# Kernel tuning notes

Measured on AMD Instinct MI355X. Metric: run time of the kernel, lower is better.

## Reference

```python
import jax, jax.numpy as jnp
import numpy as np

B_, S_, P_, D_ = 2, 512, 64, 1024
L_ = 4            # n_layer
DI_ = 2 * D_      # d_inner (expand=2)
DS_ = 16          # d_state
DC_ = 4           # d_conv
DR_ = D_ // 16    # dt_rank
PCD_ = 768        # prepend_cond_dim


def setup_inputs() -> dict:
    key = jax.random.key(0)
    ks = jax.random.split(key, 12)
    n = lambda k, s, sc=0.02: jax.random.normal(k, s, dtype=jnp.float32) * sc
    A_log = jnp.log(jnp.broadcast_to(jnp.arange(1, DS_ + 1, dtype=jnp.float32), (L_, DI_, DS_)))
    return {
        'x': jax.random.normal(ks[0], (B_, S_, D_), dtype=jnp.float32),
        'prepend_cond': jax.random.normal(ks[1], (B_, P_, PCD_), dtype=jnp.float32),
        'pre_w1': n(ks[2], (PCD_, D_)),
        'pre_w2': n(ks[3], (D_, D_)),
        'norm_w': jnp.ones((L_, D_), jnp.float32),
        'in_proj_w': n(ks[4], (L_, 2 * DI_, D_)),
        'conv_w': n(ks[5], (L_, DI_, DC_), 0.1),
        'conv_b': jnp.zeros((L_, DI_), jnp.float32),
        'x_proj_w': n(ks[6], (L_, DR_ + 2 * DS_, DI_)),
        'dt_proj_w': n(ks[7], (L_, DI_, DR_), 0.1),
        'dt_proj_b': jax.random.uniform(ks[8], (L_, DI_), jnp.float32, -4.0, -2.0),
        'A_log': A_log,
        'D_param': jnp.ones((L_, DI_), jnp.float32),
        'out_proj_w': n(ks[9], (L_, D_, DI_)),
        'final_norm_w': jnp.ones((D_,), jnp.float32),
    }


def rmsnorm(x, w, eps=1e-5):
    return x * jax.lax.rsqrt(jnp.mean(x * x, axis=-1, keepdims=True) + eps) * w


def mamba_block(x, ip_w, cw, cb, xp_w, dtp_w, dtp_b, A_log, Dp, op_w):
    B, S, _ = x.shape
    xz = jnp.einsum('bsd,ed->bse', x, ip_w)            # [B,S,2*DI]
    xi, z = jnp.split(xz, 2, axis=-1)
    # depthwise causal conv1d along time
    xt = xi.transpose(0, 2, 1)                          # [B,DI,S]
    conv = jax.lax.conv_general_dilated(
        xt, cw[:, None, :], (1,), [(DC_ - 1, 0)], feature_group_count=DI_) + cb[:, None]
    xi = jax.nn.silu(conv.transpose(0, 2, 1))           # [B,S,DI]
    xdbl = jnp.einsum('bse,fe->bsf', xi, xp_w)          # [B,S,DR+2*DS]
    dt, Bm, Cm = jnp.split(xdbl, [DR_, DR_ + DS_], axis=-1)
    dt = jax.nn.softplus(jnp.einsum('bsr,er->bse', dt, dtp_w) + dtp_b)  # [B,S,DI]
    A = -jnp.exp(A_log)                                 # [DI,DS]
    dA = jnp.exp(dt[..., None] * A)                     # [B,S,DI,DS]
    dBu = dt[..., None] * Bm[:, :, None, :] * xi[..., None]

    def step(h, t):
        da, dbu, c = t
        h = da * h + dbu                                # [B,DI,DS]
        return h, jnp.einsum('bes,bs->be', h, c)

    h0 = jnp.zeros((B, DI_, DS_), x.dtype)
    _, ys = jax.lax.scan(step, h0, (dA.transpose(1, 0, 2, 3), dBu.transpose(1, 0, 2, 3), Cm.transpose(1, 0, 2)))
    y = ys.transpose(1, 0, 2) + xi * Dp
    y = y * jax.nn.silu(z)
    return jnp.einsum('bse,de->bsd', y, op_w)


def reference(x, prepend_cond, pre_w1, pre_w2, norm_w, in_proj_w, conv_w, conv_b,
              x_proj_w, dt_proj_w, dt_proj_b, A_log, D_param, out_proj_w, final_norm_w):
    p = jax.nn.silu(prepend_cond @ pre_w1) @ pre_w2     # to_prepend_embed
    h = jnp.concatenate([p, x], axis=1)                 # [B, P+S, D]
    for l in range(L_):
        h = h + mamba_block(rmsnorm(h, norm_w[l]), in_proj_w[l], conv_w[l], conv_b[l],
                            x_proj_w[l], dt_proj_w[l], dt_proj_b[l], A_log[l],
                            D_param[l], out_proj_w[l])
    h = rmsnorm(h, final_norm_w)
    return h[:, P_:, :]
```

## Files before the change

kernel.cpp:

```cpp
#include <hip/hip_runtime.h>
#include <math.h>

#define B_ 2
#define S_ 512
#define P_ 64
#define T_ 576
#define D_ 1024
#define L_ 4
#define DI_ 2048
#define DS_ 16
#define DC_ 4
#define DR_ 64
#define PCD_ 768
#define M_ (B_*T_)
#define CCH 18
#define NC (T_/CCH)
#define XKS 16
#define OPK 4

#define N_IP (2*DI_*D_/4)
#define N_XP (96*DI_/4)
#define N_DTP (DI_*DR_/4)
#define N_OP (D_*DI_/4)
#define CVB ((N_IP + N_XP + N_DTP + N_OP + 255) / 256)
#define SETSZ ((size_t)2*DI_*D_ + 96*DI_ + DI_*DR_ + D_*DI_)

typedef __attribute__((ext_vector_type(8))) short bf16x8;
typedef __attribute__((ext_vector_type(4))) float f32x4;

__device__ __forceinline__ float silu_f(float v) { return v / (1.f + __expf(-v)); }
__device__ __forceinline__ float softplus_f(float v) {
    return fmaxf(v, 0.f) + log1pf(__expf(-fabsf(v)));
}
__device__ __forceinline__ unsigned short bf16_rne(float x) {
    unsigned int b = __float_as_uint(x);
    b += 0x7fffu + ((b >> 16) & 1u);
    return (unsigned short)(b >> 16);
}
__device__ __forceinline__ float bf16_to_f(unsigned short u) {
    return __uint_as_float((unsigned int)u << 16);
}

typedef const void __attribute__((address_space(1)))* gas_t;
typedef void __attribute__((address_space(3)))* las_t;
__device__ __forceinline__ void async16(const void* g, void* l) {
    __builtin_amdgcn_global_load_lds((gas_t)g, (las_t)l, 16, 0, 0);
}

__device__ __forceinline__ void cvt4_body(int i,
    const float* s0, unsigned short* d0, int n0,
    const float* s1, unsigned short* d1, int n1,
    const float* s2, unsigned short* d2, int n2,
    const float* s3, unsigned short* d3, int n3)
{
    const float* s; unsigned short* d; int off;
    if (i < n0)                     { s = s0; d = d0; off = i; }
    else if (i < n0 + n1)           { s = s1; d = d1; off = i - n0; }
    else if (i < n0 + n1 + n2)      { s = s2; d = d2; off = i - n0 - n1; }
    else if (i < n0 + n1 + n2 + n3) { s = s3; d = d3; off = i - n0 - n1 - n2; }
    else return;
    const float4 v = ((const float4*)s)[off];
    ushort4 o;
    o.x = bf16_rne(v.x); o.y = bf16_rne(v.y);
    o.z = bf16_rne(v.z); o.w = bf16_rne(v.w);
    ((ushort4*)d)[off] = o;
}

template<int EPI, int BN>
__global__ __launch_bounds__(256) void gemm_mfma_kernel(
    const unsigned short* __restrict__ A, const unsigned short* __restrict__ W,
    float* __restrict__ C, float* __restrict__ C2,
    int M, int N, int K, int Kchunk)
{
    constexpr int NF = BN / 32;
    __shared__ unsigned short As[128 * 32];
    __shared__ unsigned short Bs[BN * 32];
    const int tid = threadIdx.x;
    const int wave = tid >> 6;
    const int lane = tid & 63;
    const int m0 = blockIdx.y * 128, n0 = blockIdx.x * BN;
    const int kbase = blockIdx.z * Kchunk;
    const int wm = (wave >> 1) * 64, wn = (wave & 1) * (BN / 2);

    const int srow = (wave << 5) + (lane >> 2);
    const int selem = (lane & 3) * 8;
    const unsigned short* gA = A + (size_t)(m0 + srow) * K + kbase + selem;
    const unsigned short* gB = W + (size_t)(n0 + srow) * K + kbase + selem;
    unsigned short* lA = As + (wave << 5) * 32;
    unsigned short* lB = Bs + (wave << 5) * 32;

    f32x4 acc[4][NF];
    #pragma unroll
    for (int i = 0; i < 4; ++i)
        #pragma unroll
        for (int j = 0; j < NF; ++j)
            acc[i][j] = (f32x4){0.f, 0.f, 0.f, 0.f};

    const int fr = lane & 15;
    const int fq = lane >> 4;
    const int aoff = (wm + fr) * 32 + fq * 8;
    const int boff = (wn + fr) * 32 + fq * 8;

    for (int k0 = 0; k0 < Kchunk; k0 += 32) {
        async16(gA, lA);
        async16(gA + (size_t)16 * K, lA + 16 * 32);
        if (BN == 128 || wave < BN / 32) {
            async16(gB, lB);
            async16(gB + (size_t)16 * K, lB + 16 * 32);
        }
        gA += 32; gB += 32;
        __syncthreads();
        bf16x8 af[4], bf[NF];
        #pragma unroll
        for (int i = 0; i < 4; ++i) af[i] = *(const bf16x8*)&As[aoff + i * 512];
        #pragma unroll
        for (int j = 0; j < NF; ++j) bf[j] = *(const bf16x8*)&Bs[boff + j * 512];
        #pragma unroll
        for (int i = 0; i < 4; ++i)
            #pragma unroll
            for (int j = 0; j < NF; ++j)
                acc[i][j] = __builtin_amdgcn_mfma_f32_16x16x32_bf16(
                    af[i], bf[j], acc[i][j], 0, 0, 0);
        __syncthreads();
    }

    #pragma unroll
    for (int i = 0; i < 4; ++i) {
        const int m = m0 + wm + i * 16 + fq * 4;
        #pragma unroll
        for (int j = 0; j < NF; ++j) {
            const int n = n0 + wn + j * 16 + fr;
            if (EPI == 6) {
                float* p = C + ((size_t)blockIdx.z * M + m) * N + n;
                #pragma unroll
                for (int r = 0; r < 4; ++r)
                    p[(size_t)r * N] = acc[i][j][r];
            } else if (EPI == 8) {
                unsigned short* p = (unsigned short*)C +
                                    ((size_t)blockIdx.z * M + m) * N + n;
                #pragma unroll
                for (int r = 0; r < 4; ++r)
                    p[(size_t)r * N] = bf16_rne(acc[i][j][r]);
            } else if (EPI == 7) {
                if (n < DI_) {
                    unsigned short* p = (unsigned short*)C + (size_t)m * DI_ + n;
                    #pragma unroll
                    for (int r = 0; r < 4; ++r)
                        p[(size_t)r * DI_] = bf16_rne(acc[i][j][r]);
                } else {
                    unsigned short* p = (unsigned short*)C2 + (size_t)m * DI_ + (n - DI_);
                    #pragma unroll
                    for (int r = 0; r < 4; ++r)
                        p[(size_t)r * DI_] = bf16_rne(silu_f(acc[i][j][r]));
                }
            }
        }
    }
}

__global__ __launch_bounds__(256) void xproj_mfma_kernel(
    const unsigned short* __restrict__ A,
    const unsigned short* __restrict__ W,
    float* __restrict__ P)
{
    __shared__ unsigned short As[128 * 32];
    __shared__ unsigned short Bs[96 * 32];
    const int tid = threadIdx.x;
    const int wave = tid >> 6;
    const int lane = tid & 63;
    const int m0 = blockIdx.y * 128;
    const int kbase = blockIdx.x * (DI_ / XKS);
    const int wm = (wave >> 1) * 64, wn = (wave & 1) * 48;

    const int srow = (wave << 5) + (lane >> 2);
    const int selem = (lane & 3) * 8;
    const unsigned short* gA = A + (size_t)(m0 + srow) * DI_ + kbase + selem;
    const unsigned short* gB = W + (size_t)srow * DI_ + kbase + selem;
    unsigned short* lA = As + (wave << 5) * 32;
    unsigned short* lB = Bs + (wave << 5) * 32;

    f32x4 acc[4][3];
    #pragma unroll
    for (int i = 0; i < 4; ++i)
        #pragma unroll
        for (int j = 0; j < 3; ++j)
            acc[i][j] = (f32x4){0.f, 0.f, 0.f, 0.f};

    const int fr = lane & 15;
    const int fq = lane >> 4;
    const int aoff = (wm + fr) * 32 + fq * 8;
    const int boff = (wn + fr) * 32 + fq * 8;

    #pragma unroll
    for (int kk = 0; kk < 4; ++kk) {
        async16(gA, lA);
        async16(gA + (size_t)16 * DI_, lA + 16 * 32);
        if (wave < 3) {
            async16(gB, lB);
            async16(gB + (size_t)16 * DI_, lB + 16 * 32);
        }
        gA += 32; gB += 32;
        __syncthreads();
        bf16x8 af[4], bf[3];
        #pragma unroll
        for (int i = 0; i < 4; ++i) af[i] = *(const bf16x8*)&As[aoff + i * 512];
        #pragma unroll
        for (int j = 0; j < 3; ++j) bf[j] = *(const bf16x8*)&Bs[boff + j * 512];
        #pragma unroll
        for (int i = 0; i < 4; ++i)
            #pragma unroll
            for (int j = 0; j < 3; ++j)
                acc[i][j] = __builtin_amdgcn_mfma_f32_16x16x32_bf16(
                    af[i], bf[j], acc[i][j], 0, 0, 0);
        __syncthreads();
    }

    float* Pb = P + ((size_t)blockIdx.x * M_ + m0) * 96;
    #pragma unroll
    for (int i = 0; i < 4; ++i) {
        const int m = wm + i * 16 + fq * 4;
        #pragma unroll
        for (int j = 0; j < 3; ++j) {
            const int n = wn + j * 16 + fr;
            #pragma unroll
            for (int r = 0; r < 4; ++r)
                Pb[(size_t)(m + r) * 96 + n] = acc[i][j][r];
        }
    }
}

__global__ __launch_bounds__(256) void xproj_reduce_kernel(
    const float* __restrict__ P, float* __restrict__ Bc, float* __restrict__ Cc,
    unsigned short* __restrict__ dtr_bf)
{
    const int i = blockIdx.x * 256 + threadIdx.x;
    if (i >= M_ * 96) return;
    float s = 0.f;
    #pragma unroll
    for (int ks = 0; ks < XKS; ++ks) s += P[(size_t)ks * (M_ * 96) + i];
    const int m = i / 96;
    const int n = i - m * 96;
    if (n < DR_)            dtr_bf[(size_t)m * DR_ + n] = bf16_rne(s);
    else if (n < DR_ + DS_) Bc[(size_t)m * DS_ + (n - DR_)] = s;
    else                    Cc[(size_t)m * DS_ + (n - DR_ - DS_)] = s;
}

__global__ __launch_bounds__(256) void cvt_bf16_kernel(
    const float* __restrict__ in, unsigned short* __restrict__ out, int n4)
{
    const int i = blockIdx.x * 256 + threadIdx.x;
    if (i >= n4) return;
    const float4 v = ((const float4*)in)[i];
    ushort4 o;
    o.x = bf16_rne(v.x); o.y = bf16_rne(v.y);
    o.z = bf16_rne(v.z); o.w = bf16_rne(v.w);
    ((ushort4*)out)[i] = o;
}

__global__ __launch_bounds__(256) void cvt_transpose_kernel(
    const float* __restrict__ in, unsigned short* __restrict__ out, int K, int N)
{
    __shared__ float t[64][65];
    const int k0 = blockIdx.x * 64;
    const int n0 = blockIdx.y * 64;
    const int tx = threadIdx.x & 63;
    const int ty = threadIdx.x >> 6;
    #pragma unroll
    for (int j = 0; j < 16; ++j) {
        const int kk = ty * 16 + j;
        t[kk][tx] = in[(size_t)(k0 + kk) * N + n0 + tx];
    }
    __syncthreads();
    #pragma unroll
    for (int j = 0; j < 16; ++j) {
        const int nn = ty * 16 + j;
        out[(size_t)(n0 + nn) * K + k0 + tx] = bf16_rne(t[tx][nn]);
    }
}

__global__ __launch_bounds__(256) void reduce_silu_bf16_kernel(
    const float* __restrict__ P, unsigned short* __restrict__ o, int MN, int ns)
{
    const int i = blockIdx.x * 256 + threadIdx.x;
    if (i >= MN) return;
    float s = 0.f;
    for (int k = 0; k < ns; ++k) s += P[(size_t)k * MN + i];
    o[i] = bf16_rne(silu_f(s));
}
__global__ __launch_bounds__(256) void reduce_fp32_kernel(
    const float* __restrict__ P, float* __restrict__ o, int MN, int ns)
{
    const int i = blockIdx.x * 256 + threadIdx.x;
    if (i >= MN) return;
    float s = 0.f;
    for (int k = 0; k < ns; ++k) s += P[(size_t)k * MN + i];
    o[i] = s;
}

__global__ __launch_bounds__(256) void outproj_rmsnorm_cvt_kernel(
    const unsigned short* __restrict__ P, float* __restrict__ h,
    const float* __restrict__ w, unsigned short* __restrict__ outb, int donorm,
    const float* s0, unsigned short* d0, int n0,
    const float* s1, unsigned short* d1, int n1,
    const float* s2, unsigned short* d2, int n2,
    const float* s3, unsigned short* d3, int n3)
{
    const int bid = blockIdx.x;
    if (bid >= M_) {
        cvt4_body((bid - M_) * 256 + threadIdx.x,
                  s0, d0, n0, s1, d1, n1, s2, d2, n2, s3, d3, n3);
        return;
    }
    const int r = bid;
    const int i = r * 256 + threadIdx.x;
    float4 v = ((float4*)h)[i];
    #pragma unroll
    for (int k = 0; k < OPK; ++k) {
        const ushort4 a4 = ((const ushort4*)P)[(size_t)k * (M_ * D_ / 4) + i];
        v.x += bf16_to_f(a4.x); v.y += bf16_to_f(a4.y);
        v.z += bf16_to_f(a4.z); v.w += bf16_to_f(a4.w);
    }
    ((float4*)h)[i] = v;
    if (!donorm) return;
    float ss = v.x * v.x + v.y * v.y + v.z * v.z + v.w * v.w;
    ss += __shfl_xor(ss, 32, 64);
    ss += __shfl_xor(ss, 16, 64);
    ss += __shfl_xor(ss, 8, 64);
    ss += __shfl_xor(ss, 4, 64);
    ss += __shfl_xor(ss, 2, 64);
    ss += __shfl_xor(ss, 1, 64);
    __shared__ float red[4];
    if ((threadIdx.x & 63) == 0) red[threadIdx.x >> 6] = ss;
    __syncthreads();
    const float tot = red[0] + red[1] + red[2] + red[3];
    const float scale = rsqrtf(tot * (1.f / D_) + 1e-5f);
    const float4 wv = ((const float4*)w)[threadIdx.x];
    ushort4 o;
    o.x = bf16_rne(v.x * scale * wv.x);
    o.y = bf16_rne(v.y * scale * wv.y);
    o.z = bf16_rne(v.z * scale * wv.z);
    o.w = bf16_rne(v.w * scale * wv.w);
    ((ushort4*)(outb + (size_t)r * D_))[threadIdx.x] = o;
}

__global__ __launch_bounds__(256) void assemble_h_kernel(
    const float* __restrict__ p, const float* __restrict__ x, float* __restrict__ h)
{
    const int idx = blockIdx.x * 256 + threadIdx.x;
    const int r = idx >> 8;
    const int c = idx & 255;
    const int b = r / T_;
    const int t = r - b * T_;
    float4 v;
    if (t < P_) v = ((const float4*)p)[(size_t)(b * P_ + t) * 256 + c];
    else        v = ((const float4*)x)[(size_t)(b * S_ + (t - P_)) * 256 + c];
    ((float4*)h)[idx] = v;
}

__global__ __launch_bounds__(256) void rmsnorm_cvt_kernel(
    const float* __restrict__ x, const float* __restrict__ w,
    unsigned short* __restrict__ outb,
    const float* s0, unsigned short* d0, int n0,
    const float* s1, unsigned short* d1, int n1,
    const float* s2, unsigned short* d2, int n2,
    const float* s3, unsigned short* d3, int n3)
{
    const int bid = blockIdx.x;
    if (bid >= M_) {
        cvt4_body((bid - M_) * 256 + threadIdx.x,
                  s0, d0, n0, s1, d1, n1, s2, d2, n2, s3, d3, n3);
        return;
    }
    const int r = bid;
    const float4 v = ((const float4*)(x + (size_t)r * D_))[threadIdx.x];
    float ss = v.x * v.x + v.y * v.y + v.z * v.z + v.w * v.w;
    ss += __shfl_xor(ss, 32, 64);
    ss += __shfl_xor(ss, 16, 64);
    ss += __shfl_xor(ss, 8, 64);
    ss += __shfl_xor(ss, 4, 64);
    ss += __shfl_xor(ss, 2, 64);
    ss += __shfl_xor(ss, 1, 64);
    __shared__ float red[4];
    if ((threadIdx.x & 63) == 0) red[threadIdx.x >> 6] = ss;
    __syncthreads();
    const float tot = red[0] + red[1] + red[2] + red[3];
    const float scale = rsqrtf(tot * (1.f / D_) + 1e-5f);
    const float4 wv = ((const float4*)w)[threadIdx.x];
    ushort4 o;
    o.x = bf16_rne(v.x * scale * wv.x);
    o.y = bf16_rne(v.y * scale * wv.y);
    o.z = bf16_rne(v.z * scale * wv.z);
    o.w = bf16_rne(v.w * scale * wv.w);
    ((ushort4*)(outb + (size_t)r * D_))[threadIdx.x] = o;
}

__global__ __launch_bounds__(256) void final_rmsnorm_kernel(
    const float* __restrict__ h, const float* __restrict__ w, float* __restrict__ out)
{
    const int r = blockIdx.x;
    const int b = r / S_;
    const int s = r - b * S_;
    const int hr = b * T_ + P_ + s;
    const float4 v = ((const float4*)(h + (size_t)hr * D_))[threadIdx.x];
    float ss = v.x * v.x + v.y * v.y + v.z * v.z + v.w * v.w;
    ss += __shfl_xor(ss, 32, 64);
    ss += __shfl_xor(ss, 16, 64);
    ss += __shfl_xor(ss, 8, 64);
    ss += __shfl_xor(ss, 4, 64);
    ss += __shfl_xor(ss, 2, 64);
    ss += __shfl_xor(ss, 1, 64);
    __shared__ float red[4];
    if ((threadIdx.x & 63) == 0) red[threadIdx.x >> 6] = ss;
    __syncthreads();
    const float tot = red[0] + red[1] + red[2] + red[3];
    const float scale = rsqrtf(tot * (1.f / D_) + 1e-5f);
    const float4 wv = ((const float4*)w)[threadIdx.x];
    float4 o;
    o.x = v.x * scale * wv.x; o.y = v.y * scale * wv.y;
    o.z = v.z * scale * wv.z; o.w = v.w * scale * wv.w;
    ((float4*)(out + (size_t)r * D_))[threadIdx.x] = o;
}

__global__ __launch_bounds__(256) void conv_silu_kernel(
    const unsigned short* __restrict__ xb, const float* __restrict__ cw,
    const float* __restrict__ cb, unsigned short* __restrict__ xib)
{
    __shared__ float xs[67][64];
    const int tid = threadIdx.x;
    const int tx = tid & 63;
    const int ty = tid >> 6;
    const int r0 = blockIdx.x * 64;
    const int e0 = blockIdx.y * 64;
    const int bt0 = (r0 / T_) * T_;

    for (int j = ty; j < 67; j += 4) {
        const int r = r0 + j - 3;
        xs[j][tx] = (r >= bt0) ? bf16_to_f(xb[(size_t)r * DI_ + e0 + tx]) : 0.f;
    }
    __syncthreads();
    const float4 w = *(const float4*)(cw + (size_t)(e0 + tx) * 4);
    const float bias = cb[e0 + tx];
    #pragma unroll
    for (int j = 0; j < 16; ++j) {
        const int rl = ty * 16 + j;
        float v = bias;
        v = fmaf(w.x, xs[rl + 0][tx], v);
        v = fmaf(w.y, xs[rl + 1][tx], v);
        v = fmaf(w.z, xs[rl + 2][tx], v);
        v = fmaf(w.w, xs[rl + 3][tx], v);
        xib[(size_t)(r0 + rl) * DI_ + e0 + tx] = bf16_rne(silu_f(v));
    }
}

__global__ __launch_bounds__(256) void scan_chunk1_kernel(
    const unsigned short* __restrict__ dtr,
    const unsigned short* __restrict__ dtw,
    const float* __restrict__ dtbias,
    const float* __restrict__ Bc,
    const unsigned short* __restrict__ xib,
    const float* __restrict__ A_log,
    float* __restrict__ Ap, float* __restrict__ Hp)
{
    __shared__ float4 Bs[CCH][4];
    __shared__ float dtrs[CCH][DR_];
    const int tid = threadIdx.x;
    const int e = ((blockIdx.x & 7) << 8) + tid;
    const int cb = blockIdx.x >> 3;
    const int b = cb & (B_ - 1);
    const int c = cb >> 1;
    const int r0 = b * T_ + c * CCH;
    for (int i = tid; i < CCH * DS_; i += 256)
        ((float*)Bs)[i] = Bc[(size_t)r0 * DS_ + i];
    for (int i = tid; i < CCH * DR_ / 4; i += 256) {
        const ushort4 v4 = ((const ushort4*)(dtr + (size_t)r0 * DR_))[i];
        float* d = &dtrs[0][0] + i * 4;
        d[0] = bf16_to_f(v4.x); d[1] = bf16_to_f(v4.y);
        d[2] = bf16_to_f(v4.z); d[3] = bf16_to_f(v4.w);
    }
    float A2[DS_], h[DS_], a[DS_];
    const float* Ae = A_log + (size_t)e * DS_;
    #pragma unroll
    for (int s = 0; s < DS_; ++s) {
        A2[s] = -__expf(Ae[s]) * 1.44269504f;
        h[s] = 0.f; a[s] = 1.f;
    }
    __syncthreads();
    float dt[CCH];
    {
        float w[DR_];
        const ushort4* wp = (const ushort4*)(dtw + (size_t)e * DR_);
        #pragma unroll
        for (int q = 0; q < 16; ++q) {
            const ushort4 v = wp[q];
            w[q * 4 + 0] = bf16_to_f(v.x);
            w[q * 4 + 1] = bf16_to_f(v.y);
            w[q * 4 + 2] = bf16_to_f(v.z);
            w[q * 4 + 3] = bf16_to_f(v.w);
        }
        const float bb = dtbias[e];
        #pragma unroll
        for (int t = 0; t < CCH; ++t) {
            float acc = 0.f;
            #pragma unroll
            for (int r = 0; r < DR_; ++r) acc = fmaf(dtrs[t][r], w[r], acc);
            dt[t] = softplus_f(acc + bb);
        }
    }
    const unsigned short* up = xib + (size_t)r0 * DI_ + e;
    #pragma unroll
    for (int t = 0; t < CCH; ++t) {
        const float dtv = dt[t];
        const float dtu = dtv * bf16_to_f(up[(size_t)t * DI_]);
        #pragma unroll
        for (int q = 0; q < 4; ++q) {
            const float4 bq = Bs[t][q];
            const float* bb = &bq.x;
            #pragma unroll
            for (int j = 0; j < 4; ++j) {
                const int s = q * 4 + j;
                const float da = __builtin_amdgcn_exp2f(dtv * A2[s]);
                a[s] *= da;
                h[s] = fmaf(da, h[s], bb[j] * dtu);
            }
        }
    }
    const size_t o = (size_t)cb * DS_ * DI_ + e;
    #pragma unroll
    for (int s = 0; s < DS_; ++s) {
        Ap[o + (size_t)s * DI_] = a[s];
        Hp[o + (size_t)s * DI_] = h[s];
    }
}

__global__ __launch_bounds__(256) void scan_chunk2_kernel(
    float* __restrict__ Ap, float* __restrict__ Hp)
{
    const int g = blockIdx.x * 256 + threadIdx.x;
    float h = 0.f;
    #pragma unroll
    for (int c = 0; c < NC; ++c) {
        const size_t o = (size_t)c * (B_ * DI_ * DS_) + g;
        const float ap = Ap[o];
        const float hp = Hp[o];
        Hp[o] = h;
        h = fmaf(ap, h, hp);
    }
}

__global__ __launch_bounds__(256) void scan_chunk3_kernel(
    const unsigned short* __restrict__ dtr,
    const unsigned short* __restrict__ dtw,
    const float* __restrict__ dtbias,
    const float* __restrict__ Bc,
    const float* __restrict__ Cc,
    const unsigned short* __restrict__ xib,
    const unsigned short* __restrict__ szb,
    const float* __restrict__ A_log, const float* __restrict__ Dp,
    const float* __restrict__ Hin, unsigned short* __restrict__ y)
{
    __shared__ float4 Bs[CCH][4], Cs[CCH][4];
    __shared__ float dtrs[CCH][DR_];
    const int tid = threadIdx.x;
    const int e = ((blockIdx.x & 7) << 8) + tid;
    const int cb = blockIdx.x >> 3;
    const int b = cb & (B_ - 1);
    const int c = cb >> 1;
    const int r0 = b * T_ + c * CCH;
    for (int i = tid; i < CCH * DS_; i += 256) {
        ((float*)Bs)[i] = Bc[(size_t)r0 * DS_ + i];
        ((float*)Cs)[i] = Cc[(size_t)r0 * DS_ + i];
    }
    for (int i = tid; i < CCH * DR_ / 4; i += 256) {
        const ushort4 v4 = ((const ushort4*)(dtr + (size_t)r0 * DR_))[i];
        float* d = &dtrs[0][0] + i * 4;
        d[0] = bf16_to_f(v4.x); d[1] = bf16_to_f(v4.y);
        d[2] = bf16_to_f(v4.z); d[3] = bf16_to_f(v4.w);
    }
    float A2[DS_], h[DS_];
    const float* Ae = A_log + (size_t)e * DS_;
    const float dpe = Dp[e];
    const size_t ho = (size_t)cb * DS_ * DI_ + e;
    #pragma unroll
    for (int s = 0; s < DS_; ++s) {
        A2[s] = -__expf(Ae[s]) * 1.44269504f;
        h[s] = Hin[ho + (size_t)s * DI_];
    }
    __syncthreads();
    float dt[CCH];
    {
        float w[DR_];
        const ushort4* wp = (const ushort4*)(dtw + (size_t)e * DR_);
        #pragma unroll
        for (int q = 0; q < 16; ++q) {
            const ushort4 v = wp[q];
            w[q * 4 + 0] = bf16_to_f(v.x);
            w[q * 4 + 1] = bf16_to_f(v.y);
            w[q * 4 + 2] = bf16_to_f(v.z);
            w[q * 4 + 3] = bf16_to_f(v.w);
        }
        const float bb = dtbias[e];
        #pragma unroll
        for (int t = 0; t < CCH; ++t) {
            float acc = 0.f;
            #pragma unroll
            for (int r = 0; r < DR_; ++r) acc = fmaf(dtrs[t][r], w[r], acc);
            dt[t] = softplus_f(acc + bb);
        }
    }
    const unsigned short* up = xib + (size_t)r0 * DI_ + e;
    const unsigned short* sp = szb + (size_t)r0 * DI_ + e;
    unsigned short* yp = y + (size_t)r0 * DI_ + e;
    #pragma unroll
    for (int t = 0; t < CCH; ++t) {
        const float dtv = dt[t];
        const float u   = bf16_to_f(up[(size_t)t * DI_]);
        const float dtu = dtv * u;
        float y0 = 0.f, y1 = 0.f, y2 = 0.f, y3 = 0.f;
        #pragma unroll
        for (int q = 0; q < 4; ++q) {
            const float4 bq = Bs[t][q];
            const float4 cq = Cs[t][q];
            const float* bb = &bq.x;
            const float* cc = &cq.x;
            #pragma unroll
            for (int j = 0; j < 4; ++j) {
                const int s = q * 4 + j;
                const float da = __builtin_amdgcn_exp2f(dtv * A2[s]);
                h[s] = fmaf(da, h[s], bb[j] * dtu);
                if (j == 0)      y0 = fmaf(h[s], cc[j], y0);
                else if (j == 1) y1 = fmaf(h[s], cc[j], y1);
                else if (j == 2) y2 = fmaf(h[s], cc[j], y2);
                else             y3 = fmaf(h[s], cc[j], y3);
            }
        }
        const float ysum = (y0 + y1) + (y2 + y3);
        const float yv = fmaf(u, dpe, ysum) * bf16_to_f(sp[(size_t)t * DI_]);
        yp[(size_t)t * DI_] = bf16_rne(yv);
    }
}

extern "C" void kernel_launch(void* const* d_in, const int* in_sizes, int n_in,
                              void* d_out, int out_size, void* d_ws, size_t ws_size,
                              hipStream_t stream)
{
    const float* x       = (const float*)d_in[0];
    const float* pc      = (const float*)d_in[1];
    const float* pre_w1  = (const float*)d_in[2];
    const float* pre_w2  = (const float*)d_in[3];
    const float* norm_w  = (const float*)d_in[4];
    const float* ip_w    = (const float*)d_in[5];
    const float* conv_w  = (const float*)d_in[6];
    const float* conv_b  = (const float*)d_in[7];
    const float* xp_w    = (const float*)d_in[8];
    const float* dtp_w   = (const float*)d_in[9];
    const float* dtp_b   = (const float*)d_in[10];
    const float* A_log   = (const float*)d_in[11];
    const float* D_param = (const float*)d_in[12];
    const float* op_w    = (const float*)d_in[13];
    const float* fnw     = (const float*)d_in[14];
    float* out = (float*)d_out;

    float* ws = (float*)d_ws;
    float* h    = ws;  ws += (size_t)M_ * D_;
    float* xz   = ws;  ws += (size_t)M_ * 2 * DI_;
    float* scr  = ws;  ws += (size_t)M_ * DI_;
    float* Pbuf = ws;  ws += (size_t)XKS * M_ * 96;
    float* Bc   = ws;  ws += (size_t)DS_ * M_;
    float* Cc   = ws;  ws += (size_t)DS_ * M_;
    unsigned short* xn_bf  = (unsigned short*)ws;  ws += (size_t)M_ * D_ / 2;
    unsigned short* yb_bf  = (unsigned short*)ws;  ws += (size_t)M_ * DI_ / 2;
    unsigned short* xi_bf  = (unsigned short*)ws;  ws += (size_t)M_ * DI_ / 2;
    unsigned short* xb_bf  = (unsigned short*)ws;  ws += (size_t)M_ * DI_ / 2;
    unsigned short* szb_bf = (unsigned short*)ws;  ws += (size_t)M_ * DI_ / 2;
    unsigned short* dtr_bf = (unsigned short*)ws;  ws += (size_t)M_ * DR_ / 2;
    unsigned short* wsets  = (unsigned short*)ws;  ws += SETSZ;
    ws += SETSZ;

    unsigned short* ipw_b[2], *xpw_b[2], *dtpw_b[2], *opw_b[2];
    for (int s = 0; s < 2; ++s) {
        unsigned short* base = wsets + (size_t)s * SETSZ;
        ipw_b[s]  = base;
        xpw_b[s]  = base + (size_t)2 * DI_ * D_;
        dtpw_b[s] = xpw_b[s] + (size_t)96 * DI_;
        opw_b[s]  = dtpw_b[s] + (size_t)DI_ * DR_;
    }

    float* Ap = xz;
    float* Hp = xz + (size_t)NC * B_ * DI_ * DS_;

    unsigned short* pc_bf   = xi_bf;
    unsigned short* w1t_bf  = ipw_b[0];
    unsigned short* w2t_bf  = ipw_b[0] + (size_t)D_ * PCD_;
    unsigned short* tmp1_bf = xn_bf;
    float*          tmp2    = Pbuf;
    float*          P2buf   = scr;
    unsigned short* Pop     = (unsigned short*)xz;

    const dim3 blk(256);

    cvt_bf16_kernel<<<dim3(B_ * P_ * PCD_ / 4 / 256), blk, 0, stream>>>(
        pc, pc_bf, B_ * P_ * PCD_ / 4);
    cvt_transpose_kernel<<<dim3(PCD_ / 64, D_ / 64), blk, 0, stream>>>(
        pre_w1, w1t_bf, PCD_, D_);
    cvt_transpose_kernel<<<dim3(D_ / 64, D_ / 64), blk, 0, stream>>>(
        pre_w2, w2t_bf, D_, D_);
    gemm_mfma_kernel<6, 64><<<dim3(D_ / 64, 1, 12), blk, 0, stream>>>(
        pc_bf, w1t_bf, Pbuf, nullptr, B_ * P_, D_, PCD_, PCD_ / 12);
    reduce_silu_bf16_kernel<<<dim3(B_ * P_ * D_ / 256), blk, 0, stream>>>(
        Pbuf, tmp1_bf, B_ * P_ * D_, 12);
    gemm_mfma_kernel<6, 64><<<dim3(D_ / 64, 1, 16), blk, 0, stream>>>(
        tmp1_bf, w2t_bf, P2buf, nullptr, B_ * P_, D_, D_, D_ / 16);
    reduce_fp32_kernel<<<dim3(B_ * P_ * D_ / 256), blk, 0, stream>>>(
        P2buf, tmp2, B_ * P_ * D_, 16);
    assemble_h_kernel<<<dim3(M_ * D_ / 4 / 256), blk, 0, stream>>>(tmp2, x, h);

    rmsnorm_cvt_kernel<<<dim3(M_ + CVB), blk, 0, stream>>>(
        h, norm_w, xn_bf,
        ip_w, ipw_b[0], N_IP,
        xp_w, xpw_b[0], N_XP,
        dtp_w, dtpw_b[0], N_DTP,
        op_w, opw_b[0], N_OP);

    for (int l = 0; l < L_; ++l) {
        const int s = l & 1;
        gemm_mfma_kernel<7, 64><<<dim3(2 * DI_ / 64, M_ / 128, 1), blk, 0, stream>>>(
            xn_bf, ipw_b[s], (float*)xb_bf, (float*)szb_bf, M_, 2 * DI_, D_, D_);
        conv_silu_kernel<<<dim3(M_ / 64, DI_ / 64), blk, 0, stream>>>(
            xb_bf, conv_w + (size_t)l * DI_ * DC_, conv_b + (size_t)l * DI_,
            xi_bf);
        xproj_mfma_kernel<<<dim3(XKS, M_ / 128), blk, 0, stream>>>(
            xi_bf, xpw_b[s], Pbuf);
        xproj_reduce_kernel<<<dim3((M_ * 96 + 255) / 256), blk, 0, stream>>>(
            Pbuf, Bc, Cc, dtr_bf);
        scan_chunk1_kernel<<<dim3(NC * B_ * DI_ / 256), blk, 0, stream>>>(
            dtr_bf, dtpw_b[s], dtp_b + (size_t)l * DI_, Bc, xi_bf,
            A_log + (size_t)l * DI_ * DS_, Ap, Hp);
        scan_chunk2_kernel<<<dim3(B_ * DI_ * DS_ / 256), blk, 0, stream>>>(Ap, Hp);
        scan_chunk3_kernel<<<dim3(NC * B_ * DI_ / 256), blk, 0, stream>>>(
            dtr_bf, dtpw_b[s], dtp_b + (size_t)l * DI_, Bc, Cc, xi_bf, szb_bf,
            A_log + (size_t)l * DI_ * DS_, D_param + (size_t)l * DI_, Hp, yb_bf);
        gemm_mfma_kernel<8, 64><<<dim3(D_ / 64, M_ / 128, OPK), blk, 0, stream>>>(
            yb_bf, opw_b[s], (float*)Pop, nullptr, M_, D_, DI_, DI_ / OPK);
        const int docvt = (l + 1 < L_);
        outproj_rmsnorm_cvt_kernel<<<dim3(M_ + (docvt ? CVB : 0)), blk, 0, stream>>>(
            Pop, h, norm_w + (size_t)((l + 1) & 3) * D_, xn_bf, l < L_ - 1,
            ip_w + (size_t)(l + 1) * 2 * DI_ * D_, ipw_b[s ^ 1], docvt ? N_IP : 0,
            xp_w + (size_t)(l + 1) * 96 * DI_, xpw_b[s ^ 1], docvt ? N_XP : 0,
            dtp_w + (size_t)(l + 1) * DI_ * DR_, dtpw_b[s ^ 1], docvt ? N_DTP : 0,
            op_w + (size_t)(l + 1) * D_ * DI_, opw_b[s ^ 1], docvt ? N_OP : 0);
    }

    final_rmsnorm_kernel<<<dim3(B_ * S_), blk, 0, stream>>>(h, fnw, out);
}
```

Baseline: 673.9 us.

## Double-buffer LDS tiles in the MFMA GEMM and x_proj kernels

```diff
diff --git a/kernel.cpp b/kernel.cpp
--- a/kernel.cpp
+++ b/kernel.cpp
@@ -73,8 +73,8 @@
     int M, int N, int K, int Kchunk)
 {
     constexpr int NF = BN / 32;
-    __shared__ unsigned short As[128 * 32];
-    __shared__ unsigned short Bs[BN * 32];
+    __shared__ unsigned short As[2][128 * 32];
+    __shared__ unsigned short Bs[2][BN * 32];
     const int tid = threadIdx.x;
     const int wave = tid >> 6;
     const int lane = tid & 63;
@@ -86,8 +86,7 @@
     const int selem = (lane & 3) * 8;
     const unsigned short* gA = A + (size_t)(m0 + srow) * K + kbase + selem;
     const unsigned short* gB = W + (size_t)(n0 + srow) * K + kbase + selem;
-    unsigned short* lA = As + (wave << 5) * 32;
-    unsigned short* lB = Bs + (wave << 5) * 32;
+    const int lofs = (wave << 5) * 32;
 
     f32x4 acc[4][NF];
     #pragma unroll
@@ -101,20 +100,29 @@
     const int aoff = (wm + fr) * 32 + fq * 8;
     const int boff = (wn + fr) * 32 + fq * 8;
 
-    for (int k0 = 0; k0 < Kchunk; k0 += 32) {
-        async16(gA, lA);
-        async16(gA + (size_t)16 * K, lA + 16 * 32);
-        if (BN == 128 || wave < BN / 32) {
-            async16(gB, lB);
-            async16(gB + (size_t)16 * K, lB + 16 * 32);
-        }
-        gA += 32; gB += 32;
-        __syncthreads();
+    const int NT = Kchunk >> 5;
+
+    #define STAGE(b, t) do {                                              \
+        const unsigned short* pA = gA + (t) * 32;                         \
+        async16(pA, &As[b][lofs]);                                        \
+        async16(pA + (size_t)16 * K, &As[b][lofs + 16 * 32]);             \
+        if (BN == 128 || wave < BN / 32) {                                \
+            const unsigned short* pB = gB + (t) * 32;                     \
+            async16(pB, &Bs[b][lofs]);                                    \
+            async16(pB + (size_t)16 * K, &Bs[b][lofs + 16 * 32]);         \
+        }                                                                 \
+    } while (0)
+
+    STAGE(0, 0);
+    __syncthreads();
+    for (int t = 0; t < NT; ++t) {
+        const int cur = t & 1;
+        if (t + 1 < NT) STAGE(cur ^ 1, t + 1);
         bf16x8 af[4], bf[NF];
         #pragma unroll
-        for (int i = 0; i < 4; ++i) af[i] = *(const bf16x8*)&As[aoff + i * 512];
-        #pragma unroll
-        for (int j = 0; j < NF; ++j) bf[j] = *(const bf16x8*)&Bs[boff + j * 512];
+        for (int i = 0; i < 4; ++i) af[i] = *(const bf16x8*)&As[cur][aoff + i * 512];
+        #pragma unroll
+        for (int j = 0; j < NF; ++j) bf[j] = *(const bf16x8*)&Bs[cur][boff + j * 512];
         #pragma unroll
         for (int i = 0; i < 4; ++i)
             #pragma unroll
@@ -123,6 +131,7 @@
                     af[i], bf[j], acc[i][j], 0, 0, 0);
         __syncthreads();
     }
+    #undef STAGE
 
     #pragma unroll
     for (int i = 0; i < 4; ++i) {
@@ -163,8 +172,8 @@
     const unsigned short* __restrict__ W,
     float* __restrict__ P)
 {
-    __shared__ unsigned short As[128 * 32];
-    __shared__ unsigned short Bs[96 * 32];
+    __shared__ unsigned short As[2][128 * 32];
+    __shared__ unsigned short Bs[2][96 * 32];
     const int tid = threadIdx.x;
     const int wave = tid >> 6;
     const int lane = tid & 63;
@@ -176,8 +185,7 @@
     const int selem = (lane & 3) * 8;
     const unsigned short* gA = A + (size_t)(m0 + srow) * DI_ + kbase + selem;
     const unsigned short* gB = W + (size_t)srow * DI_ + kbase + selem;
-    unsigned short* lA = As + (wave << 5) * 32;
-    unsigned short* lB = Bs + (wave << 5) * 32;
+    const int lofs = (wave << 5) * 32;
 
     f32x4 acc[4][3];
     #pragma unroll
@@ -191,21 +199,28 @@
     const int aoff = (wm + fr) * 32 + fq * 8;
     const int boff = (wn + fr) * 32 + fq * 8;
 
-    #pragma unroll
-    for (int kk = 0; kk < 4; ++kk) {
-        async16(gA, lA);
-        async16(gA + (size_t)16 * DI_, lA + 16 * 32);
-        if (wave < 3) {
-            async16(gB, lB);
-            async16(gB + (size_t)16 * DI_, lB + 16 * 32);
-        }
-        gA += 32; gB += 32;
-        __syncthreads();
+    #define XSTAGE(b, t) do {                                             \
+        const unsigned short* pA = gA + (t) * 32;                         \
+        async16(pA, &As[b][lofs]);                                        \
+        async16(pA + (size_t)16 * DI_, &As[b][lofs + 16 * 32]);           \
+        if (wave < 3) {                                                   \
+            const unsigned short* pB = gB + (t) * 32;                     \
+            async16(pB, &Bs[b][lofs]);                                    \
+            async16(pB + (size_t)16 * DI_, &Bs[b][lofs + 16 * 32]);       \
+        }                                                                 \
+    } while (0)
+
+    XSTAGE(0, 0);
+    __syncthreads();
+    #pragma unroll
+    for (int t = 0; t < 4; ++t) {
+        const int cur = t & 1;
+        if (t + 1 < 4) XSTAGE(cur ^ 1, t + 1);
         bf16x8 af[4], bf[3];
         #pragma unroll
-        for (int i = 0; i < 4; ++i) af[i] = *(const bf16x8*)&As[aoff + i * 512];
-        #pragma unroll
-        for (int j = 0; j < 3; ++j) bf[j] = *(const bf16x8*)&Bs[boff + j * 512];
+        for (int i = 0; i < 4; ++i) af[i] = *(const bf16x8*)&As[cur][aoff + i * 512];
+        #pragma unroll
+        for (int j = 0; j < 3; ++j) bf[j] = *(const bf16x8*)&Bs[cur][boff + j * 512];
         #pragma unroll
         for (int i = 0; i < 4; ++i)
             #pragma unroll
@@ -214,6 +229,7 @@
                     af[i], bf[j], acc[i][j], 0, 0, 0);
         __syncthreads();
     }
+    #undef XSTAGE
 
     float* Pb = P + ((size_t)blockIdx.x * M_ + m0) * 96;
     #pragma unroll
```

New measurement: 667.1 us. Within noise of the previous version (-1.0%).
